# Optimization experiments

Measured on AMD Instinct MI355X. Metric: run time of the kernel, lower is better.

## Reference

```python
import jax, jax.numpy as jnp
import numpy as np

B, N, D, H = 8, 2048, 512, 8  # graphs, nodes/graph, d_model, n_heads
DH = D // H


def setup_inputs() -> dict:
    key = jax.random.key(0)
    ks = jax.random.split(key, 9)
    def lin_w(k):
        return jax.random.normal(k, (D, D), jnp.float32) * (D ** -0.5)
    def lin_b(k):
        return jax.random.normal(k, (D,), jnp.float32) * 0.01
    return {
        "x": jax.random.normal(ks[0], (B * N, D), jnp.float32),
        # equal-size, sorted segments -> to_dense_batch is a pure reshape, mask all-true
        "batch": jnp.repeat(jnp.arange(B, dtype=jnp.int32), N),
        "n_graphs": B,
        "Wq": lin_w(ks[1]), "bq": lin_b(ks[2]),
        "Wk": lin_w(ks[3]), "bk": lin_b(ks[4]),
        "Wv": lin_w(ks[5]), "bv": lin_b(ks[6]),
        "Wo": lin_w(ks[7]), "bo": lin_b(ks[8]),
    }


def reference(x, batch, n_graphs, Wq, bq, Wk, bk, Wv, bv, Wo, bo):
    total, d = x.shape
    n = total // n_graphs
    scaling = (d // H) ** -0.5
    # to_dense_batch with equal-size sorted segments == reshape; mask is all True
    xd = x.reshape(n_graphs, n, d)                      # [b, n, d]
    # Linear layers (torch: y = x @ W.T + b)
    q = (xd @ Wq.T + bq).reshape(n_graphs, n, H, DH)    # [b, n, h, x]
    k = (xd @ Wk.T + bk).reshape(n_graphs, n, H, DH)
    v = (xd @ Wv.T + bv).reshape(n_graphs, n, H, DH)
    # NOTE (faithful to source): scores[b,h,i,j] = K_i . Q_j ; softmax over j (query axis)
    scores = jnp.einsum('bihx,bjhx->bhij', k, q) * scaling  # [b, h, n, n]
    attn = jax.nn.softmax(scores, axis=-1)
    out = jnp.einsum('bhij,bjhx->bihx', attn, v)            # [b, n, h, x]
    out = out.reshape(n_graphs, n, d)                       # concat heads
    out = out @ Wo.T + bo                                   # final linear
    return out.reshape(total, d)                            # out_dense[mask] (all-true mask)
```

## Files before the change

kernel.cpp:

```cpp
#include <hip/hip_runtime.h>
#include <hip/hip_bf16.h>
#include <stdint.h>

#define BB 8
#define NN 2048
#define DD 512
#define HH 8
#define DHH 64
#define TOTAL (BB*NN)

typedef __attribute__((ext_vector_type(8))) short short8_t;
typedef __attribute__((ext_vector_type(4))) float float4_t;

__device__ __forceinline__ unsigned short f32_bf16(float f) {
    union { float f; unsigned int u; } v; v.f = f;
    unsigned int u = v.u + 0x7FFFu + ((v.u >> 16) & 1u);
    return (unsigned short)(u >> 16);
}

__device__ __forceinline__ unsigned int cvt_pk_bf16(float a, float b) {
    unsigned int r;
    asm("v_cvt_pk_bf16_f32 %0, %1, %2" : "=v"(r) : "v"(a), "v"(b));
    return r;
}

__device__ __forceinline__ float exp2_hw(float x) {
    return __builtin_amdgcn_exp2f(x);
}

#define KSCALE 0.1803368801f
#define PBIAS  17.3123404907f

__global__ __launch_bounds__(256)
void xprep(const float* __restrict__ x, unsigned short* __restrict__ xb)
{
    size_t i8 = ((size_t)blockIdx.x * 256 + threadIdx.x) * 8;
    float4 a = *(const float4*)(x + i8);
    float4 b = *(const float4*)(x + i8 + 4);
    uint4 s;
    s.x = cvt_pk_bf16(a.x, a.y);
    s.y = cvt_pk_bf16(a.z, a.w);
    s.z = cvt_pk_bf16(b.x, b.y);
    s.w = cvt_pk_bf16(b.z, b.w);
    *(uint4*)(xb + i8) = s;
}

#define LDA 40

__global__ __launch_bounds__(256, 2)
void qkv_gemm(const unsigned short* __restrict__ xb,
              const float* __restrict__ Wq, const float* __restrict__ bq,
              const float* __restrict__ Wk, const float* __restrict__ bk,
              const float* __restrict__ Wv, const float* __restrict__ bv,
              unsigned short* __restrict__ q_buf,
              unsigned short* __restrict__ k_buf,
              unsigned short* __restrict__ v_buf)
{
    __shared__ __align__(16) unsigned short As[128*LDA];
    __shared__ __align__(16) unsigned short Bs[128*LDA];

    const int which = blockIdx.z;
    const float* W    = (which==0) ? Wq : ((which==1) ? Wk : Wv);
    const float* bias = (which==0) ? bq : ((which==1) ? bk : bv);

    const int m0 = blockIdx.x * 128;
    const int n0 = blockIdx.y * 128;
    const int t  = threadIdx.x;
    const int lane = t & 63;
    const int w  = t >> 6;
    const int wm = w >> 1, wn = w & 1;
    const int c  = lane & 15, qd = lane >> 4;

    float4_t acc[4][4];
    #pragma unroll
    for (int i = 0; i < 4; i++)
        #pragma unroll
        for (int j = 0; j < 4; j++) acc[i][j] = (float4_t){0.f,0.f,0.f,0.f};

    for (int k0 = 0; k0 < DD; k0 += 32) {
        __syncthreads();
        #pragma unroll
        for (int p = 0; p < 2; p++) {
            int ci = p*256 + t;
            int row = ci >> 2, c8 = (ci & 3) << 3;
            *(int4*)(As + row*LDA + c8) = *(const int4*)(xb + (size_t)(m0+row)*DD + k0 + c8);
        }
        #pragma unroll
        for (int p = 0; p < 4; p++) {
            int ci = p*256 + t;
            int row = ci >> 3, c4 = (ci & 7) << 2;
            float4 wv = *(const float4*)(W + (size_t)(n0+row)*DD + k0 + c4);
            uint2 w16;
            w16.x = cvt_pk_bf16(wv.x, wv.y);
            w16.y = cvt_pk_bf16(wv.z, wv.w);
            *(uint2*)(Bs + row*LDA + c4) = w16;
        }
        __syncthreads();

        short8_t af[4], bf[4];
        #pragma unroll
        for (int ti = 0; ti < 4; ti++)
            af[ti] = *(const short8_t*)(As + (wm*64 + ti*16 + c)*LDA + qd*8);
        #pragma unroll
        for (int tj = 0; tj < 4; tj++)
            bf[tj] = *(const short8_t*)(Bs + (wn*64 + tj*16 + c)*LDA + qd*8);
        #pragma unroll
        for (int ti = 0; ti < 4; ti++)
            #pragma unroll
            for (int tj = 0; tj < 4; tj++)
                acc[ti][tj] = __builtin_amdgcn_mfma_f32_16x16x32_bf16(af[ti], bf[tj], acc[ti][tj], 0, 0, 0);
    }

    #pragma unroll
    for (int tj = 0; tj < 4; tj++) {
        int dcol = n0 + wn*64 + tj*16 + c;
        float bval = bias[dcol];
        int h = dcol >> 6, xf = dcol & 63;
        #pragma unroll
        for (int ti = 0; ti < 4; ti++) {
            #pragma unroll
            for (int r = 0; r < 4; r++) {
                int gm = m0 + wm*64 + ti*16 + qd*4 + r;
                int b_ = gm >> 11, n_ = gm & 2047;
                float val = acc[ti][tj][r] + bval;
                if (which == 1) val *= KSCALE;
                unsigned short o16 = f32_bf16(val);
                if (which == 2)
                    v_buf[(size_t)((b_*HH + h)*DHH + xf)*NN + n_] = o16;
                else if (which == 0)
                    q_buf[(size_t)((b_*HH + h)*NN + n_)*DHH + xf] = o16;
                else
                    k_buf[(size_t)((b_*HH + h)*NN + n_)*DHH + xf] = o16;
            }
        }
    }
}

#define LDK 68

__global__ __launch_bounds__(256, 4)
void flash_attn(const unsigned short* __restrict__ q_buf,
                const unsigned short* __restrict__ v_buf,
                unsigned short* __restrict__ ko)
{
    __shared__ __align__(16) unsigned short KPs[128*LDK];
    __shared__ __align__(16) unsigned short Qs[64*LDK];
    __shared__ __align__(16) unsigned short Vs[80*LDK];

    const int bh = blockIdx.x;
    const int i0 = blockIdx.y * 128;
    unsigned short* KOg = ko + (size_t)bh*NN*DHH;
    const unsigned short* Qg = q_buf + (size_t)bh*NN*DHH;
    const unsigned short* Vg = v_buf + (size_t)bh*DHH*NN;

    const int t = threadIdx.x;
    const int lane = t & 63, w = t >> 6;
    const int c = lane & 15, qd = lane >> 4;
    const int sr = t >> 3;
    const int sc = (t & 7) << 3;

    #pragma unroll
    for (int p = 0; p < 4; p++) {
        int ci = p*256 + t;
        int row = ci >> 3, c8 = (ci & 7) << 3;
        *(int4*)(KPs + row*LDK + c8) = *(const int4*)(KOg + (size_t)(i0+row)*DHH + c8);
    }
    *(int4*)(Qs + sr*LDK + sc)      = *(const int4*)(Qg + (size_t)sr*DHH + sc);
    *(int4*)(Qs + (sr+32)*LDK + sc) = *(const int4*)(Qg + (size_t)(sr+32)*DHH + sc);
    *(int4*)(Vs + sr*LDK + sc)      = *(const int4*)(Vg + (size_t)sr*NN + sc);
    *(int4*)(Vs + (sr+32)*LDK + sc) = *(const int4*)(Vg + (size_t)(sr+32)*NN + sc);
    for (int q0 = t; q0 < 16*LDK; q0 += 256) {
        int row = 64 + q0 / LDK, col = q0 % LDK;
        Vs[row*LDK + col] = (row == 64) ? (unsigned short)0x3F80 : (unsigned short)0;
    }
    __syncthreads();

    short8_t afK[2][2];
    #pragma unroll
    for (int it = 0; it < 2; it++)
        #pragma unroll
        for (int xs = 0; xs < 2; xs++)
            afK[it][xs] = *(const short8_t*)(KPs + (w*32 + it*16 + c)*LDK + xs*32 + qd*8);

    float4_t oacc[2][5];
    #pragma unroll
    for (int it = 0; it < 2; it++)
        #pragma unroll
        for (int xt = 0; xt < 5; xt++) oacc[it][xt] = (float4_t){0.f,0.f,0.f,0.f};

    for (int j0 = 0; j0 < NN; j0 += 64) {
        int jn = (j0 + 64) & (NN - 1);
        int4 qn0 = *(const int4*)(Qg + (size_t)(jn + sr)*DHH + sc);
        int4 qn1 = *(const int4*)(Qg + (size_t)(jn + sr + 32)*DHH + sc);
        int4 vn0 = *(const int4*)(Vg + (size_t)sr*NN + jn + sc);
        int4 vn1 = *(const int4*)(Vg + (size_t)(sr+32)*NN + jn + sc);

        float4_t sacc[2][4];
        #pragma unroll
        for (int it = 0; it < 2; it++)
            #pragma unroll
            for (int jt = 0; jt < 4; jt++)
                sacc[it][jt] = (float4_t){-PBIAS,-PBIAS,-PBIAS,-PBIAS};
        #pragma unroll
        for (int jt = 0; jt < 4; jt++)
            #pragma unroll
            for (int xs = 0; xs < 2; xs++) {
                short8_t bq_ = *(const short8_t*)(Qs + (jt*16 + c)*LDK + xs*32 + qd*8);
                sacc[0][jt] = __builtin_amdgcn_mfma_f32_16x16x32_bf16(afK[0][xs], bq_, sacc[0][jt], 0, 0, 0);
                sacc[1][jt] = __builtin_amdgcn_mfma_f32_16x16x32_bf16(afK[1][xs], bq_, sacc[1][jt], 0, 0, 0);
            }

        #pragma unroll
        for (int it = 0; it < 2; it++)
            #pragma unroll
            for (int jt = 0; jt < 4; jt++) {
                float p0 = exp2_hw(sacc[it][jt][0]);
                float p1 = exp2_hw(sacc[it][jt][1]);
                float p2 = exp2_hw(sacc[it][jt][2]);
                float p3 = exp2_hw(sacc[it][jt][3]);
                unsigned int d0 = cvt_pk_bf16(p0, p1);
                unsigned int d1 = cvt_pk_bf16(p2, p3);
                int base = (w*32 + it*16 + qd*4)*LDK + jt*16 + c;
                KPs[base        ] = (unsigned short)d0;
                KPs[base +   LDK] = (unsigned short)(d0 >> 16);
                KPs[base + 2*LDK] = (unsigned short)d1;
                KPs[base + 3*LDK] = (unsigned short)(d1 >> 16);
            }

        short8_t afP[2][2];
        #pragma unroll
        for (int it = 0; it < 2; it++)
            #pragma unroll
            for (int ks = 0; ks < 2; ks++)
                afP[it][ks] = *(const short8_t*)(KPs + (w*32 + it*16 + c)*LDK + ks*32 + qd*8);

        #pragma unroll
        for (int xt = 0; xt < 5; xt++)
            #pragma unroll
            for (int ks = 0; ks < 2; ks++) {
                short8_t bv_ = *(const short8_t*)(Vs + (xt*16 + c)*LDK + ks*32 + qd*8);
                oacc[0][xt] = __builtin_amdgcn_mfma_f32_16x16x32_bf16(afP[0][ks], bv_, oacc[0][xt], 0, 0, 0);
                oacc[1][xt] = __builtin_amdgcn_mfma_f32_16x16x32_bf16(afP[1][ks], bv_, oacc[1][xt], 0, 0, 0);
            }

        __syncthreads();
        *(int4*)(Qs + sr*LDK + sc)      = qn0;
        *(int4*)(Qs + (sr+32)*LDK + sc) = qn1;
        *(int4*)(Vs + sr*LDK + sc)      = vn0;
        *(int4*)(Vs + (sr+32)*LDK + sc) = vn1;
        __syncthreads();
    }

    #pragma unroll
    for (int it = 0; it < 2; it++) {
        float inv[4];
        #pragma unroll
        for (int r = 0; r < 4; r++) {
            float l = __shfl(oacc[it][4][r], lane & 48, 64);
            inv[r] = 1.0f / l;
        }
        #pragma unroll
        for (int xt = 0; xt < 4; xt++)
            #pragma unroll
            for (int r = 0; r < 4; r++) {
                int i_loc = w*32 + it*16 + qd*4 + r;
                KOg[(size_t)(i0 + i_loc)*DHH + xt*16 + c] = f32_bf16(oacc[it][xt][r] * inv[r]);
            }
    }
}

__global__ __launch_bounds__(256, 2)
void out_gemm(const unsigned short* __restrict__ o_hm,
              const float* __restrict__ Wo, const float* __restrict__ bo,
              float* __restrict__ fin)
{
    __shared__ __align__(16) unsigned short As[128*LDA];
    __shared__ __align__(16) unsigned short Bs[128*LDA];

    const int m0 = blockIdx.x * 128;
    const int n0 = blockIdx.y * 128;
    const int t  = threadIdx.x;
    const int lane = t & 63;
    const int w  = t >> 6;
    const int wm = w >> 1, wn = w & 1;
    const int c  = lane & 15, qd = lane >> 4;

    const int b_ = m0 >> 11;
    const int nr = m0 & 2047;

    float4_t acc[4][4];
    #pragma unroll
    for (int i = 0; i < 4; i++)
        #pragma unroll
        for (int j = 0; j < 4; j++) acc[i][j] = (float4_t){0.f,0.f,0.f,0.f};

    for (int k0 = 0; k0 < DD; k0 += 32) {
        const int h_ = k0 >> 6;
        const int x0 = k0 & 63;
        const unsigned short* Abase = o_hm + ((size_t)(b_*HH + h_)*NN + nr)*DHH + x0;
        __syncthreads();
        #pragma unroll
        for (int p = 0; p < 2; p++) {
            int ci = p*256 + t;
            int row = ci >> 2, c8 = (ci & 3) << 3;
            *(int4*)(As + row*LDA + c8) = *(const int4*)(Abase + (size_t)row*DHH + c8);
        }
        #pragma unroll
        for (int p = 0; p < 4; p++) {
            int ci = p*256 + t;
            int row = ci >> 3, c4 = (ci & 7) << 2;
            float4 wv = *(const float4*)(Wo + (size_t)(n0+row)*DD + k0 + c4);
            uint2 w16;
            w16.x = cvt_pk_bf16(wv.x, wv.y);
            w16.y = cvt_pk_bf16(wv.z, wv.w);
            *(uint2*)(Bs + row*LDA + c4) = w16;
        }
        __syncthreads();

        short8_t af[4], bf[4];
        #pragma unroll
        for (int ti = 0; ti < 4; ti++)
            af[ti] = *(const short8_t*)(As + (wm*64 + ti*16 + c)*LDA + qd*8);
        #pragma unroll
        for (int tj = 0; tj < 4; tj++)
            bf[tj] = *(const short8_t*)(Bs + (wn*64 + tj*16 + c)*LDA + qd*8);
        #pragma unroll
        for (int ti = 0; ti < 4; ti++)
            #pragma unroll
            for (int tj = 0; tj < 4; tj++)
                acc[ti][tj] = __builtin_amdgcn_mfma_f32_16x16x32_bf16(af[ti], bf[tj], acc[ti][tj], 0, 0, 0);
    }

    #pragma unroll
    for (int tj = 0; tj < 4; tj++) {
        int dcol = n0 + wn*64 + tj*16 + c;
        float bval = bo[dcol];
        #pragma unroll
        for (int ti = 0; ti < 4; ti++) {
            #pragma unroll
            for (int r = 0; r < 4; r++) {
                int gm = m0 + wm*64 + ti*16 + qd*4 + r;
                fin[(size_t)gm*DD + dcol] = acc[ti][tj][r] + bval;
            }
        }
    }
}

extern "C" void kernel_launch(void* const* d_in, const int* in_sizes, int n_in,
                              void* d_out, int out_size, void* d_ws, size_t ws_size,
                              hipStream_t stream)
{
    const float* x  = (const float*)d_in[0];
    const float* Wq = (const float*)d_in[3];  const float* bq = (const float*)d_in[4];
    const float* Wk = (const float*)d_in[5];  const float* bk = (const float*)d_in[6];
    const float* Wv = (const float*)d_in[7];  const float* bv = (const float*)d_in[8];
    const float* Wo = (const float*)d_in[9];  const float* bo = (const float*)d_in[10];

    const size_t SEG  = (size_t)TOTAL * DD * sizeof(unsigned short);
    const size_t need = 4096 + 2*SEG;
    if (ws_size < need) return;

    unsigned short* v_ws  = (unsigned short*)((char*)d_ws + 4096);
    unsigned short* ko_ws = (unsigned short*)((char*)d_ws + 4096 + SEG);
    unsigned short* q_buf = (unsigned short*)d_out;
    unsigned short* xb    = (unsigned short*)((char*)d_out + SEG);
    float* fin = (float*)d_out;

    xprep<<<dim3(TOTAL*DD/(256*8)), 256, 0, stream>>>(x, xb);
    qkv_gemm<<<dim3(TOTAL/128, DD/128, 3), 256, 0, stream>>>(
        xb, Wq, bq, Wk, bk, Wv, bv, q_buf, ko_ws, v_ws);
    flash_attn<<<dim3(BB*HH, NN/128), 256, 0, stream>>>(q_buf, v_ws, ko_ws);
    out_gemm<<<dim3(TOTAL/128, DD/128), 256, 0, stream>>>(ko_ws, Wo, bo, fin);
}
```

Before: 289.1 us.

## Pre-convert weights to bf16 and stage GEMM tiles via direct global-to-LDS loads

```diff
diff --git a/kernel.cpp b/kernel.cpp
--- a/kernel.cpp
+++ b/kernel.cpp
@@ -26,6 +26,13 @@
 
 __device__ __forceinline__ float exp2_hw(float x) {
     return __builtin_amdgcn_exp2f(x);
+}
+
+__device__ __forceinline__ void gl2lds16(const void* g, void* l) {
+    __builtin_amdgcn_global_load_lds(
+        (const __attribute__((address_space(1))) unsigned int*)g,
+        (__attribute__((address_space(3))) unsigned int*)l,
+        16, 0, 0);
 }
 
 #define KSCALE 0.1803368801f
@@ -45,22 +52,39 @@
     *(uint4*)(xb + i8) = s;
 }
 
-#define LDA 40
-
-__global__ __launch_bounds__(256, 2)
-void qkv_gemm(const unsigned short* __restrict__ xb,
-              const float* __restrict__ Wq, const float* __restrict__ bq,
-              const float* __restrict__ Wk, const float* __restrict__ bk,
-              const float* __restrict__ Wv, const float* __restrict__ bv,
-              unsigned short* __restrict__ q_buf,
-              unsigned short* __restrict__ k_buf,
-              unsigned short* __restrict__ v_buf)
-{
-    __shared__ __align__(16) unsigned short As[128*LDA];
-    __shared__ __align__(16) unsigned short Bs[128*LDA];
+__global__ __launch_bounds__(256)
+void wprep(const float* __restrict__ Wq, const float* __restrict__ Wk,
+           const float* __restrict__ Wv, const float* __restrict__ Wo,
+           unsigned short* __restrict__ w16)
+{
+    const float* src = (blockIdx.y==0) ? Wq : (blockIdx.y==1) ? Wk
+                     : (blockIdx.y==2) ? Wv : Wo;
+    unsigned short* dst = w16 + (size_t)blockIdx.y * DD * DD;
+    size_t i8 = ((size_t)blockIdx.x * 256 + threadIdx.x) * 8;
+    float4 a = *(const float4*)(src + i8);
+    float4 b = *(const float4*)(src + i8 + 4);
+    uint4 s;
+    s.x = cvt_pk_bf16(a.x, a.y);
+    s.y = cvt_pk_bf16(a.z, a.w);
+    s.z = cvt_pk_bf16(b.x, b.y);
+    s.w = cvt_pk_bf16(b.z, b.w);
+    *(uint4*)(dst + i8) = s;
+}
+
+__global__ __launch_bounds__(256, 3)
+void qkv_gemm_f(const unsigned short* __restrict__ xb,
+                const unsigned short* __restrict__ w16,
+                const float* __restrict__ bq, const float* __restrict__ bk,
+                const float* __restrict__ bv,
+                unsigned short* __restrict__ q_buf,
+                unsigned short* __restrict__ k_buf,
+                unsigned short* __restrict__ v_buf)
+{
+    __shared__ __align__(16) unsigned short As[128*32];
+    __shared__ __align__(16) unsigned short Bs[128*32];
 
     const int which = blockIdx.z;
-    const float* W    = (which==0) ? Wq : ((which==1) ? Wk : Wv);
+    const unsigned short* W = w16 + (size_t)which * DD * DD;
     const float* bias = (which==0) ? bq : ((which==1) ? bk : bv);
 
     const int m0 = blockIdx.x * 128;
@@ -71,6 +95,13 @@
     const int wm = w >> 1, wn = w & 1;
     const int c  = lane & 15, qd = lane >> 4;
 
+    const int srow = t >> 2;
+    const int scol = (t & 3) << 3;
+    unsigned short* AsB0 = As + (size_t)(w*64)*8;
+    unsigned short* AsB1 = As + (size_t)(256 + w*64)*8;
+    unsigned short* BsB0 = Bs + (size_t)(w*64)*8;
+    unsigned short* BsB1 = Bs + (size_t)(256 + w*64)*8;
+
     float4_t acc[4][4];
     #pragma unroll
     for (int i = 0; i < 4; i++)
@@ -79,31 +110,19 @@
 
     for (int k0 = 0; k0 < DD; k0 += 32) {
         __syncthreads();
-        #pragma unroll
-        for (int p = 0; p < 2; p++) {
-            int ci = p*256 + t;
-            int row = ci >> 2, c8 = (ci & 3) << 3;
-            *(int4*)(As + row*LDA + c8) = *(const int4*)(xb + (size_t)(m0+row)*DD + k0 + c8);
-        }
-        #pragma unroll
-        for (int p = 0; p < 4; p++) {
-            int ci = p*256 + t;
-            int row = ci >> 3, c4 = (ci & 7) << 2;
-            float4 wv = *(const float4*)(W + (size_t)(n0+row)*DD + k0 + c4);
-            uint2 w16;
-            w16.x = cvt_pk_bf16(wv.x, wv.y);
-            w16.y = cvt_pk_bf16(wv.z, wv.w);
-            *(uint2*)(Bs + row*LDA + c4) = w16;
-        }
+        gl2lds16(xb + (size_t)(m0 + srow)*DD      + k0 + scol, AsB0);
+        gl2lds16(xb + (size_t)(m0 + 64 + srow)*DD + k0 + scol, AsB1);
+        gl2lds16(W  + (size_t)(n0 + srow)*DD      + k0 + scol, BsB0);
+        gl2lds16(W  + (size_t)(n0 + 64 + srow)*DD + k0 + scol, BsB1);
         __syncthreads();
 
         short8_t af[4], bf[4];
         #pragma unroll
         for (int ti = 0; ti < 4; ti++)
-            af[ti] = *(const short8_t*)(As + (wm*64 + ti*16 + c)*LDA + qd*8);
+            af[ti] = *(const short8_t*)(As + (wm*64 + ti*16 + c)*32 + qd*8);
         #pragma unroll
         for (int tj = 0; tj < 4; tj++)
-            bf[tj] = *(const short8_t*)(Bs + (wn*64 + tj*16 + c)*LDA + qd*8);
+            bf[tj] = *(const short8_t*)(Bs + (wn*64 + tj*16 + c)*32 + qd*8);
         #pragma unroll
         for (int ti = 0; ti < 4; ti++)
             #pragma unroll
@@ -136,6 +155,97 @@
     }
 }
 
+#define LDA 40
+
+__global__ __launch_bounds__(256, 2)
+void qkv_gemm(const unsigned short* __restrict__ xb,
+              const float* __restrict__ Wq, const float* __restrict__ bq,
+              const float* __restrict__ Wk, const float* __restrict__ bk,
+              const float* __restrict__ Wv, const float* __restrict__ bv,
+              unsigned short* __restrict__ q_buf,
+              unsigned short* __restrict__ k_buf,
+              unsigned short* __restrict__ v_buf)
+{
+    __shared__ __align__(16) unsigned short As[128*LDA];
+    __shared__ __align__(16) unsigned short Bs[128*LDA];
+
+    const int which = blockIdx.z;
+    const float* W    = (which==0) ? Wq : ((which==1) ? Wk : Wv);
+    const float* bias = (which==0) ? bq : ((which==1) ? bk : bv);
+
+    const int m0 = blockIdx.x * 128;
+    const int n0 = blockIdx.y * 128;
+    const int t  = threadIdx.x;
+    const int lane = t & 63;
+    const int w  = t >> 6;
+    const int wm = w >> 1, wn = w & 1;
+    const int c  = lane & 15, qd = lane >> 4;
+
+    float4_t acc[4][4];
+    #pragma unroll
+    for (int i = 0; i < 4; i++)
+        #pragma unroll
+        for (int j = 0; j < 4; j++) acc[i][j] = (float4_t){0.f,0.f,0.f,0.f};
+
+    for (int k0 = 0; k0 < DD; k0 += 32) {
+        __syncthreads();
+        #pragma unroll
+        for (int p = 0; p < 2; p++) {
+            int ci = p*256 + t;
+            int row = ci >> 2, c8 = (ci & 3) << 3;
+            *(int4*)(As + row*LDA + c8) = *(const int4*)(xb + (size_t)(m0+row)*DD + k0 + c8);
+        }
+        #pragma unroll
+        for (int p = 0; p < 4; p++) {
+            int ci = p*256 + t;
+            int row = ci >> 3, c4 = (ci & 7) << 2;
+            float4 wv = *(const float4*)(W + (size_t)(n0+row)*DD + k0 + c4);
+            uint2 w16v;
+            w16v.x = cvt_pk_bf16(wv.x, wv.y);
+            w16v.y = cvt_pk_bf16(wv.z, wv.w);
+            *(uint2*)(Bs + row*LDA + c4) = w16v;
+        }
+        __syncthreads();
+
+        short8_t af[4], bf[4];
+        #pragma unroll
+        for (int ti = 0; ti < 4; ti++)
+            af[ti] = *(const short8_t*)(As + (wm*64 + ti*16 + c)*LDA + qd*8);
+        #pragma unroll
+        for (int tj = 0; tj < 4; tj++)
+            bf[tj] = *(const short8_t*)(Bs + (wn*64 + tj*16 + c)*LDA + qd*8);
+        #pragma unroll
+        for (int ti = 0; ti < 4; ti++)
+            #pragma unroll
+            for (int tj = 0; tj < 4; tj++)
+                acc[ti][tj] = __builtin_amdgcn_mfma_f32_16x16x32_bf16(af[ti], bf[tj], acc[ti][tj], 0, 0, 0);
+    }
+
+    #pragma unroll
+    for (int tj = 0; tj < 4; tj++) {
+        int dcol = n0 + wn*64 + tj*16 + c;
+        float bval = bias[dcol];
+        int h = dcol >> 6, xf = dcol & 63;
+        #pragma unroll
+        for (int ti = 0; ti < 4; ti++) {
+            #pragma unroll
+            for (int r = 0; r < 4; r++) {
+                int gm = m0 + wm*64 + ti*16 + qd*4 + r;
+                int b_ = gm >> 11, n_ = gm & 2047;
+                float val = acc[ti][tj][r] + bval;
+                if (which == 1) val *= KSCALE;
+                unsigned short o16 = f32_bf16(val);
+                if (which == 2)
+                    v_buf[(size_t)((b_*HH + h)*DHH + xf)*NN + n_] = o16;
+                else if (which == 0)
+                    q_buf[(size_t)((b_*HH + h)*NN + n_)*DHH + xf] = o16;
+                else
+                    k_buf[(size_t)((b_*HH + h)*NN + n_)*DHH + xf] = o16;
+            }
+        }
+    }
+}
+
 #define LDK 68
 
 __global__ __launch_bounds__(256, 4)
@@ -269,13 +379,14 @@
     }
 }
 
-__global__ __launch_bounds__(256, 2)
-void out_gemm(const unsigned short* __restrict__ o_hm,
-              const float* __restrict__ Wo, const float* __restrict__ bo,
-              float* __restrict__ fin)
-{
-    __shared__ __align__(16) unsigned short As[128*LDA];
-    __shared__ __align__(16) unsigned short Bs[128*LDA];
+__global__ __launch_bounds__(256, 3)
+void out_gemm_f(const unsigned short* __restrict__ o_hm,
+                const unsigned short* __restrict__ Wo16,
+                const float* __restrict__ bo,
+                float* __restrict__ fin)
+{
+    __shared__ __align__(16) unsigned short As[128*32];
+    __shared__ __align__(16) unsigned short Bs[128*32];
 
     const int m0 = blockIdx.x * 128;
     const int n0 = blockIdx.y * 128;
@@ -288,6 +399,13 @@
     const int b_ = m0 >> 11;
     const int nr = m0 & 2047;
 
+    const int srow = t >> 2;
+    const int scol = (t & 3) << 3;
+    unsigned short* AsB0 = As + (size_t)(w*64)*8;
+    unsigned short* AsB1 = As + (size_t)(256 + w*64)*8;
+    unsigned short* BsB0 = Bs + (size_t)(w*64)*8;
+    unsigned short* BsB1 = Bs + (size_t)(256 + w*64)*8;
+
     float4_t acc[4][4];
     #pragma unroll
     for (int i = 0; i < 4; i++)
@@ -299,6 +417,71 @@
         const int x0 = k0 & 63;
         const unsigned short* Abase = o_hm + ((size_t)(b_*HH + h_)*NN + nr)*DHH + x0;
         __syncthreads();
+        gl2lds16(Abase + (size_t)srow*DHH        + scol, AsB0);
+        gl2lds16(Abase + (size_t)(64 + srow)*DHH + scol, AsB1);
+        gl2lds16(Wo16 + (size_t)(n0 + srow)*DD      + k0 + scol, BsB0);
+        gl2lds16(Wo16 + (size_t)(n0 + 64 + srow)*DD + k0 + scol, BsB1);
+        __syncthreads();
+
+        short8_t af[4], bf[4];
+        #pragma unroll
+        for (int ti = 0; ti < 4; ti++)
+            af[ti] = *(const short8_t*)(As + (wm*64 + ti*16 + c)*32 + qd*8);
+        #pragma unroll
+        for (int tj = 0; tj < 4; tj++)
+            bf[tj] = *(const short8_t*)(Bs + (wn*64 + tj*16 + c)*32 + qd*8);
+        #pragma unroll
+        for (int ti = 0; ti < 4; ti++)
+            #pragma unroll
+            for (int tj = 0; tj < 4; tj++)
+                acc[ti][tj] = __builtin_amdgcn_mfma_f32_16x16x32_bf16(af[ti], bf[tj], acc[ti][tj], 0, 0, 0);
+    }
+
+    #pragma unroll
+    for (int tj = 0; tj < 4; tj++) {
+        int dcol = n0 + wn*64 + tj*16 + c;
+        float bval = bo[dcol];
+        #pragma unroll
+        for (int ti = 0; ti < 4; ti++) {
+            #pragma unroll
+            for (int r = 0; r < 4; r++) {
+                int gm = m0 + wm*64 + ti*16 + qd*4 + r;
+                fin[(size_t)gm*DD + dcol] = acc[ti][tj][r] + bval;
+            }
+        }
+    }
+}
+
+__global__ __launch_bounds__(256, 2)
+void out_gemm(const unsigned short* __restrict__ o_hm,
+              const float* __restrict__ Wo, const float* __restrict__ bo,
+              float* __restrict__ fin)
+{
+    __shared__ __align__(16) unsigned short As[128*LDA];
+    __shared__ __align__(16) unsigned short Bs[128*LDA];
+
+    const int m0 = blockIdx.x * 128;
+    const int n0 = blockIdx.y * 128;
+    const int t  = threadIdx.x;
+    const int lane = t & 63;
+    const int w  = t >> 6;
+    const int wm = w >> 1, wn = w & 1;
+    const int c  = lane & 15, qd = lane >> 4;
+
+    const int b_ = m0 >> 11;
+    const int nr = m0 & 2047;
+
+    float4_t acc[4][4];
+    #pragma unroll
+    for (int i = 0; i < 4; i++)
+        #pragma unroll
+        for (int j = 0; j < 4; j++) acc[i][j] = (float4_t){0.f,0.f,0.f,0.f};
+
+    for (int k0 = 0; k0 < DD; k0 += 32) {
+        const int h_ = k0 >> 6;
+        const int x0 = k0 & 63;
+        const unsigned short* Abase = o_hm + ((size_t)(b_*HH + h_)*NN + nr)*DHH + x0;
+        __syncthreads();
         #pragma unroll
         for (int p = 0; p < 2; p++) {
             int ci = p*256 + t;
@@ -310,10 +493,10 @@
             int ci = p*256 + t;
             int row = ci >> 3, c4 = (ci & 7) << 2;
             float4 wv = *(const float4*)(Wo + (size_t)(n0+row)*DD + k0 + c4);
-            uint2 w16;
-            w16.x = cvt_pk_bf16(wv.x, wv.y);
-            w16.y = cvt_pk_bf16(wv.z, wv.w);
-            *(uint2*)(Bs + row*LDA + c4) = w16;
+            uint2 w16v;
+            w16v.x = cvt_pk_bf16(wv.x, wv.y);
+            w16v.y = cvt_pk_bf16(wv.z, wv.w);
+            *(uint2*)(Bs + row*LDA + c4) = w16v;
         }
         __syncthreads();
 
@@ -356,19 +539,34 @@
     const float* Wv = (const float*)d_in[7];  const float* bv = (const float*)d_in[8];
     const float* Wo = (const float*)d_in[9];  const float* bo = (const float*)d_in[10];
 
-    const size_t SEG  = (size_t)TOTAL * DD * sizeof(unsigned short);
-    const size_t need = 4096 + 2*SEG;
+    const size_t SEG   = (size_t)TOTAL * DD * sizeof(unsigned short);
+    const size_t W16SZ = (size_t)4 * DD * DD * sizeof(unsigned short);
+    const size_t need  = 4096 + 2*SEG;
+    const size_t need2 = need + W16SZ;
     if (ws_size < need) return;
+    const bool fast = (ws_size >= need2);
 
     unsigned short* v_ws  = (unsigned short*)((char*)d_ws + 4096);
     unsigned short* ko_ws = (unsigned short*)((char*)d_ws + 4096 + SEG);
+    unsigned short* w16   = (unsigned short*)((char*)d_ws + 4096 + 2*SEG);
     unsigned short* q_buf = (unsigned short*)d_out;
     unsigned short* xb    = (unsigned short*)((char*)d_out + SEG);
     float* fin = (float*)d_out;
 
     xprep<<<dim3(TOTAL*DD/(256*8)), 256, 0, stream>>>(x, xb);
-    qkv_gemm<<<dim3(TOTAL/128, DD/128, 3), 256, 0, stream>>>(
-        xb, Wq, bq, Wk, bk, Wv, bv, q_buf, ko_ws, v_ws);
+    if (fast) {
+        wprep<<<dim3(DD*DD/(256*8), 4), 256, 0, stream>>>(Wq, Wk, Wv, Wo, w16);
+        qkv_gemm_f<<<dim3(TOTAL/128, DD/128, 3), 256, 0, stream>>>(
+            xb, w16, bq, bk, bv, q_buf, ko_ws, v_ws);
+    } else {
+        qkv_gemm<<<dim3(TOTAL/128, DD/128, 3), 256, 0, stream>>>(
+            xb, Wq, bq, Wk, bk, Wv, bv, q_buf, ko_ws, v_ws);
+    }
     flash_attn<<<dim3(BB*HH, NN/128), 256, 0, stream>>>(q_buf, v_ws, ko_ws);
-    out_gemm<<<dim3(TOTAL/128, DD/128), 256, 0, stream>>>(ko_ws, Wo, bo, fin);
-}
+    if (fast) {
+        out_gemm_f<<<dim3(TOTAL/128, DD/128), 256, 0, stream>>>(
+            ko_ws, w16 + (size_t)3*DD*DD, bo, fin);
+    } else {
+        out_gemm<<<dim3(TOTAL/128, DD/128), 256, 0, stream>>>(ko_ws, Wo, bo, fin);
+    }
+}
```

Result: faster. 279.4 us (-3.3%).
